# Optimization experiments

Hardware: AMD Instinct MI355X
Metric: run time of the kernel (lower is better)

Reference implementation:

```python
import jax, jax.numpy as jnp
import numpy as np

IN, OUT, RANK, ALPHA, GS = 4096, 4096, 16, 32, 64
SCALING = ALPHA / RANK  # alpha / rank = 2.0


def setup_inputs() -> dict:
    key = jax.random.key(0)
    k1, k2, k3, k4, k5 = jax.random.split(key, 5)
    x = jax.random.normal(k1, (4, 2048, IN), dtype=jnp.float32)
    # signed int4 codes in [-8, 7]
    q_w = jax.random.randint(k2, (OUT, IN), -8, 8, dtype=jnp.int32)
    # per-group absmax scales (positive, small)
    scales = jax.random.uniform(k3, (OUT, IN // GS), dtype=jnp.float32) * 0.02 + 1e-3
    lora_A = jax.random.normal(k4, (RANK, IN), dtype=jnp.float32) * 0.02
    lora_B = jax.random.normal(k5, (OUT, RANK), dtype=jnp.float32) * 0.02
    return {"x": x, "q_w": q_w, "scales": scales, "lora_A": lora_A, "lora_B": lora_B}


def reference(x, q_w, scales, lora_A, lora_B):
    # Dequantize 4-bit base weight: blockwise symmetric, group_size=GS along in_features.
    # W[o, g*GS + j] = q[o, g*GS + j] * scales[o, g]
    W = (q_w.astype(jnp.float32).reshape(OUT, IN // GS, GS)
         * scales[:, :, None]).reshape(OUT, IN)
    # Frozen base layer: y = x @ W^T (Linear4bit, no bias)
    base_output = jnp.einsum('bsi,oi->bso', x, W)
    # LoRA branch (dropout p=0 -> identity): B(A(x)) * (alpha/rank)
    lora_output = jnp.einsum('bsr,or->bso', jnp.einsum('bsi,ri->bsr', x, lora_A), lora_B) * SCALING
    return base_output + lora_output
```

## Files before the change

### kernel.cpp

```cpp
#include <hip/hip_runtime.h>
#include <hip/hip_bf16.h>


typedef unsigned short u16;
typedef __attribute__((ext_vector_type(8))) short bf16x8;
typedef __attribute__((ext_vector_type(4))) float f32x4;
typedef __attribute__((ext_vector_type(4))) int i32x4;

#define M_DIM 8192
#define N_DIM 4096
#define K_DIM 4096
#define BK 64
#define KT_MAIN 64
#define NT 65

__device__ static inline u16 f2bf(float f) {
    union { float f; unsigned u; } v; v.f = f;
    unsigned r = v.u + 0x7fffu + ((v.u >> 16) & 1u);
    return (u16)(r >> 16);
}

__device__ static inline void gload16(const void* g, void* s) {
    __builtin_amdgcn_global_load_lds(
        (const __attribute__((address_space(1))) void*)g,
        (__attribute__((address_space(3))) void*)s, 16, 0, 0);
}

__global__ __launch_bounds__(256) void wprep_kernel(
        const int* __restrict__ q, const float* __restrict__ scales,
        u16* __restrict__ Wb) {
    int idx = blockIdx.x * 256 + threadIdx.x;
    int o  = idx >> 9;
    int kc = (idx & 511) << 3;
    float s = scales[(o << 6) + (kc >> 6)];
    const i32x4* qp = (const i32x4*)(q + (size_t)o * K_DIM + kc);
    i32x4 q0 = __builtin_nontemporal_load(qp);
    i32x4 q1 = __builtin_nontemporal_load(qp + 1);
    ushort4 r0, r1;
    r0.x = f2bf((float)q0.x * s); r0.y = f2bf((float)q0.y * s);
    r0.z = f2bf((float)q0.z * s); r0.w = f2bf((float)q0.w * s);
    r1.x = f2bf((float)q1.x * s); r1.y = f2bf((float)q1.y * s);
    r1.z = f2bf((float)q1.z * s); r1.w = f2bf((float)q1.w * s);
    *(ushort4*)&Wb[(size_t)o * K_DIM + kc]     = r0;
    *(ushort4*)&Wb[(size_t)o * K_DIM + kc + 4] = r1;
}

__global__ __launch_bounds__(256) void bprep_kernel(
        const float* __restrict__ lora_B, u16* __restrict__ B2) {
    int idx = blockIdx.x * 256 + threadIdx.x;
    int o = idx >> 6, r = idx & 63;
    B2[idx] = (r < 16) ? f2bf(lora_B[o * 16 + r]) : (u16)0;
}

__global__ __launch_bounds__(256) void xprep_kernel(
        const float* __restrict__ x, const float* __restrict__ lora_A,
        u16* __restrict__ xb, u16* __restrict__ t2) {
    const int tid = threadIdx.x, w = tid >> 6, l = tid & 63;
    const int rb = blockIdx.x * 8 + w * 2;
    float acc[2][16];
#pragma unroll
    for (int j = 0; j < 2; ++j)
#pragma unroll
        for (int r = 0; r < 16; ++r) acc[j][r] = 0.f;

    for (int i = 0; i < 16; ++i) {
        int k0 = i * 256 + l * 4;
        f32x4 x0 = __builtin_nontemporal_load(
                        (const f32x4*)&x[(size_t)rb * K_DIM + k0]);
        f32x4 x1 = __builtin_nontemporal_load(
                        (const f32x4*)&x[(size_t)(rb + 1) * K_DIM + k0]);
        ushort4 o0, o1;
        o0.x = f2bf(x0.x); o0.y = f2bf(x0.y); o0.z = f2bf(x0.z); o0.w = f2bf(x0.w);
        o1.x = f2bf(x1.x); o1.y = f2bf(x1.y); o1.z = f2bf(x1.z); o1.w = f2bf(x1.w);
        *(ushort4*)&xb[(size_t)rb * K_DIM + k0]       = o0;
        *(ushort4*)&xb[(size_t)(rb + 1) * K_DIM + k0] = o1;
#pragma unroll
        for (int r = 0; r < 16; ++r) {
            f32x4 av = *(const f32x4*)&lora_A[(size_t)r * K_DIM + k0];
            acc[0][r] += x0.x * av.x + x0.y * av.y + x0.z * av.z + x0.w * av.w;
            acc[1][r] += x1.x * av.x + x1.y * av.y + x1.z * av.z + x1.w * av.w;
        }
    }
#pragma unroll
    for (int j = 0; j < 2; ++j)
#pragma unroll
        for (int r = 0; r < 16; ++r) {
            float v = acc[j][r];
            v += __shfl_xor(v, 32); v += __shfl_xor(v, 16);
            v += __shfl_xor(v, 8);  v += __shfl_xor(v, 4);
            v += __shfl_xor(v, 2);  v += __shfl_xor(v, 1);
            acc[j][r] = v;
        }
    float lo = 0.f, hi = 0.f;
#pragma unroll
    for (int j = 0; j < 2; ++j)
#pragma unroll
        for (int c = 0; c < 8; ++c)
            if (l == j * 32 + c) { lo = acc[j][2 * c]; hi = acc[j][2 * c + 1]; }
    unsigned pack = (unsigned)f2bf(2.0f * lo) | ((unsigned)f2bf(2.0f * hi) << 16);
    *(unsigned*)&t2[(size_t)(rb + (l >> 5)) * 64 + (l & 31) * 2] = pack;
}

__global__ __launch_bounds__(512, 2) void qlora_gemm(
        const u16* __restrict__ xb, const u16* __restrict__ Wb,
        const u16* __restrict__ t2, const u16* __restrict__ B2,
        float* __restrict__ out) {
    __shared__ u16 lds[2][32768];
    int bid = blockIdx.x;
    int swz = (bid & 7) * 64 + (bid >> 3);
    int bn = swz >> 5;
    int bm = swz & 31;
    const int tid = threadIdx.x, w = tid >> 6, l = tid & 63;
    const int wr = w >> 2, wc = w & 3;
    const int fr = l & 15, fq = l >> 4;
    const int s0 = fq ^ (fr & 7);

    const int sw16 = ((l & 7) ^ ((l >> 3) & 7)) << 4;
    const int rl   = w * 8 + (l >> 3);
    size_t offA[4], offB[4], lOffA[4], lOffB[4];
#pragma unroll
    for (int o = 0; o < 4; ++o) {
        int rA = bm * 256 + o * 64 + rl;
        int rB = bn * 256 + o * 64 + rl;
        offA[o]  = (size_t)rA * 8192 + sw16;
        offB[o]  = (size_t)rB * 8192 + sw16;
        lOffA[o] = (size_t)rA * 128 + sw16;
        lOffB[o] = (size_t)rB * 128 + sw16;
    }
    char* ldsC = (char*)&lds[0][0];
    const int dst = w * 1024 + l * 16;

    const int arow = (wr * 128 + fr) * 128;
    const int brow = 32768 + (wc * 64 + fr) * 128;

    f32x4 acc[8][4] = {};

    auto stage = [&](int kt, int buf) {
        char* base = ldsC + buf * 65536;
        if (kt < KT_MAIN) {
            size_t ko = (size_t)kt * 128;
#pragma unroll
            for (int o = 0; o < 4; ++o) {
                gload16((const char*)xb + offA[o] + ko, base + dst + o * 8192);
                gload16((const char*)Wb + offB[o] + ko, base + 32768 + dst + o * 8192);
            }
        } else {
#pragma unroll
            for (int o = 0; o < 4; ++o) {
                gload16((const char*)t2 + lOffA[o], base + dst + o * 8192);
                gload16((const char*)B2 + lOffB[o], base + 32768 + dst + o * 8192);
            }
        }
    };

    stage(0, 0);
    asm volatile("s_waitcnt vmcnt(0)" ::: "memory");
    __builtin_amdgcn_s_barrier();
    asm volatile("" ::: "memory");

    for (int t = 0; t < NT; ++t) {
        const char* cb = ldsC + (t & 1) * 65536;
        if (t + 1 < NT) stage(t + 1, (t + 1) & 1);

        bf16x8 a0[8], b0[4];
#pragma unroll
        for (int j = 0; j < 4; ++j)
            b0[j] = *(const bf16x8*)(cb + brow + j * 2048 + s0 * 16);
#pragma unroll
        for (int i = 0; i < 8; ++i)
            a0[i] = *(const bf16x8*)(cb + arow + i * 2048 + s0 * 16);
        __builtin_amdgcn_s_setprio(1);
#pragma unroll
        for (int i = 0; i < 8; ++i)
#pragma unroll
            for (int j = 0; j < 4; ++j)
                acc[i][j] = __builtin_amdgcn_mfma_f32_16x16x32_bf16(
                                a0[i], b0[j], acc[i][j], 0, 0, 0);
        __builtin_amdgcn_s_setprio(0);

        bf16x8 a1[8], b1[4];
#pragma unroll
        for (int j = 0; j < 4; ++j)
            b1[j] = *(const bf16x8*)(cb + brow + j * 2048 + (s0 ^ 4) * 16);
#pragma unroll
        for (int i = 0; i < 8; ++i)
            a1[i] = *(const bf16x8*)(cb + arow + i * 2048 + (s0 ^ 4) * 16);
        __builtin_amdgcn_s_setprio(1);
#pragma unroll
        for (int i = 0; i < 8; ++i)
#pragma unroll
            for (int j = 0; j < 4; ++j)
                acc[i][j] = __builtin_amdgcn_mfma_f32_16x16x32_bf16(
                                a1[i], b1[j], acc[i][j], 0, 0, 0);
        __builtin_amdgcn_s_setprio(0);

        if (t + 1 < NT) {
            asm volatile("s_waitcnt vmcnt(0)" ::: "memory");
            __builtin_amdgcn_s_barrier();
            asm volatile("" ::: "memory");
        }
    }

    float* obase = out + (size_t)(bm * 256 + wr * 128 + fq * 4) * N_DIM
                       + bn * 256 + wc * 64 + fr;
#pragma unroll
    for (int i = 0; i < 8; ++i)
#pragma unroll
        for (int j = 0; j < 4; ++j)
#pragma unroll
            for (int r = 0; r < 4; ++r)
                obase[(size_t)(i * 16 + r) * N_DIM + j * 16] = acc[i][j][r];
}

extern "C" void kernel_launch(void* const* d_in, const int* in_sizes, int n_in,
                              void* d_out, int out_size, void* d_ws, size_t ws_size,
                              hipStream_t stream) {
    const float* x      = (const float*)d_in[0];
    const int*   qw     = (const int*)d_in[1];
    const float* scales = (const float*)d_in[2];
    const float* lora_A = (const float*)d_in[3];
    const float* lora_B = (const float*)d_in[4];
    float* out = (float*)d_out;

    char* ws = (char*)d_ws;
    u16* xb = (u16*)(ws);
    u16* Wb = (u16*)(ws + 67108864);
    u16* t2 = (u16*)(ws + 100663296);
    u16* B2 = (u16*)(ws + 101711872);

    wprep_kernel<<<8192, 256, 0, stream>>>(qw, scales, Wb);
    bprep_kernel<<<1024, 256, 0, stream>>>(lora_B, B2);
    xprep_kernel<<<1024, 256, 0, stream>>>(x, lora_A, xb, t2);
    qlora_gemm<<<dim3(512), 512, 0, stream>>>(xb, Wb, t2, B2, out);
}
```

Before: 322.0 us.

## Software-pipeline LDS fragment reads across K halves and barrier

```diff
diff --git a/kernel.cpp b/kernel.cpp
--- a/kernel.cpp
+++ b/kernel.cpp
@@ -117,16 +117,8 @@
 
     const int sw16 = ((l & 7) ^ ((l >> 3) & 7)) << 4;
     const int rl   = w * 8 + (l >> 3);
-    size_t offA[4], offB[4], lOffA[4], lOffB[4];
-#pragma unroll
-    for (int o = 0; o < 4; ++o) {
-        int rA = bm * 256 + o * 64 + rl;
-        int rB = bn * 256 + o * 64 + rl;
-        offA[o]  = (size_t)rA * 8192 + sw16;
-        offB[o]  = (size_t)rB * 8192 + sw16;
-        lOffA[o] = (size_t)rA * 128 + sw16;
-        lOffB[o] = (size_t)rB * 128 + sw16;
-    }
+    const int rA0  = bm * 256 + rl;
+    const int rB0  = bn * 256 + rl;
     char* ldsC = (char*)&lds[0][0];
     const int dst = w * 1024 + l * 16;
 
@@ -141,14 +133,18 @@
             size_t ko = (size_t)kt * 128;
 #pragma unroll
             for (int o = 0; o < 4; ++o) {
-                gload16((const char*)xb + offA[o] + ko, base + dst + o * 8192);
-                gload16((const char*)Wb + offB[o] + ko, base + 32768 + dst + o * 8192);
+                gload16((const char*)xb + ((size_t)(rA0 + o * 64) * 8192 + sw16) + ko,
+                        base + dst + o * 8192);
+                gload16((const char*)Wb + ((size_t)(rB0 + o * 64) * 8192 + sw16) + ko,
+                        base + 32768 + dst + o * 8192);
             }
         } else {
 #pragma unroll
             for (int o = 0; o < 4; ++o) {
-                gload16((const char*)t2 + lOffA[o], base + dst + o * 8192);
-                gload16((const char*)B2 + lOffB[o], base + 32768 + dst + o * 8192);
+                gload16((const char*)t2 + ((size_t)(rA0 + o * 64) * 128 + sw16),
+                        base + dst + o * 8192);
+                gload16((const char*)B2 + ((size_t)(rB0 + o * 64) * 128 + sw16),
+                        base + 32768 + dst + o * 8192);
             }
         }
     };
@@ -158,17 +154,26 @@
     __builtin_amdgcn_s_barrier();
     asm volatile("" ::: "memory");
 
+    bf16x8 a0[8], b0[4], a1[8], b1[4];
+#pragma unroll
+    for (int j = 0; j < 4; ++j)
+        b0[j] = *(const bf16x8*)(ldsC + brow + j * 2048 + s0 * 16);
+#pragma unroll
+    for (int i = 0; i < 8; ++i)
+        a0[i] = *(const bf16x8*)(ldsC + arow + i * 2048 + s0 * 16);
+
     for (int t = 0; t < NT; ++t) {
         const char* cb = ldsC + (t & 1) * 65536;
+
+#pragma unroll
+        for (int j = 0; j < 4; ++j)
+            b1[j] = *(const bf16x8*)(cb + brow + j * 2048 + (s0 ^ 4) * 16);
+#pragma unroll
+        for (int i = 0; i < 8; ++i)
+            a1[i] = *(const bf16x8*)(cb + arow + i * 2048 + (s0 ^ 4) * 16);
         if (t + 1 < NT) stage(t + 1, (t + 1) & 1);
-
-        bf16x8 a0[8], b0[4];
-#pragma unroll
-        for (int j = 0; j < 4; ++j)
-            b0[j] = *(const bf16x8*)(cb + brow + j * 2048 + s0 * 16);
-#pragma unroll
-        for (int i = 0; i < 8; ++i)
-            a0[i] = *(const bf16x8*)(cb + arow + i * 2048 + s0 * 16);
+        __builtin_amdgcn_sched_barrier(0);
+
         __builtin_amdgcn_s_setprio(1);
 #pragma unroll
         for (int i = 0; i < 8; ++i)
@@ -177,14 +182,24 @@
                 acc[i][j] = __builtin_amdgcn_mfma_f32_16x16x32_bf16(
                                 a0[i], b0[j], acc[i][j], 0, 0, 0);
         __builtin_amdgcn_s_setprio(0);
-
-        bf16x8 a1[8], b1[4];
-#pragma unroll
-        for (int j = 0; j < 4; ++j)
-            b1[j] = *(const bf16x8*)(cb + brow + j * 2048 + (s0 ^ 4) * 16);
-#pragma unroll
-        for (int i = 0; i < 8; ++i)
-            a1[i] = *(const bf16x8*)(cb + arow + i * 2048 + (s0 ^ 4) * 16);
+        __builtin_amdgcn_sched_barrier(0);
+
+        asm volatile("s_waitcnt lgkmcnt(0)" ::: "memory");
+        asm volatile("s_waitcnt vmcnt(0)" ::: "memory");
+        __builtin_amdgcn_s_barrier();
+        asm volatile("" ::: "memory");
+
+        if (t + 1 < NT) {
+            const char* nb = ldsC + ((t + 1) & 1) * 65536;
+#pragma unroll
+            for (int j = 0; j < 4; ++j)
+                b0[j] = *(const bf16x8*)(nb + brow + j * 2048 + s0 * 16);
+#pragma unroll
+            for (int i = 0; i < 8; ++i)
+                a0[i] = *(const bf16x8*)(nb + arow + i * 2048 + s0 * 16);
+        }
+        __builtin_amdgcn_sched_barrier(0);
+
         __builtin_amdgcn_s_setprio(1);
 #pragma unroll
         for (int i = 0; i < 8; ++i)
@@ -193,12 +208,7 @@
                 acc[i][j] = __builtin_amdgcn_mfma_f32_16x16x32_bf16(
                                 a1[i], b1[j], acc[i][j], 0, 0, 0);
         __builtin_amdgcn_s_setprio(0);
-
-        if (t + 1 < NT) {
-            asm volatile("s_waitcnt vmcnt(0)" ::: "memory");
-            __builtin_amdgcn_s_barrier();
-            asm volatile("" ::: "memory");
-        }
+        __builtin_amdgcn_sched_barrier(0);
     }
 
     float* obase = out + (size_t)(bm * 256 + wr * 128 + fq * 4) * N_DIM
```

Result: faster. 313.3 us (-2.7%).
